# Optimization experiments

Hardware: AMD Instinct MI355X
Metric: run time of the kernel (lower is better)

The kernel has to match this reference:

```python
import jax, jax.numpy as jnp
import numpy as np

BLANK = 0          # tf.nn.ctc_loss default blank_index (StringLookup reserves 0 for OOV)
PAD = 127          # padding_value = char_to_num.vocabulary_size()
NEG = -1e30        # log-space 'zero' (avoid -inf to keep grads NaN-free)
B, T, C, L = 1024, 256, 128, 32


def setup_inputs() -> dict:
    key = jax.random.key(0)
    k1, k2 = jax.random.split(key)
    # labels in [1, PAD-1]; none equal PAD so label_length == L (full-length labels)
    y_true = jax.random.randint(k1, (B, L), 1, PAD).astype(jnp.int32)
    y_pred = jax.random.normal(k2, (B, T, C), dtype=jnp.float32)
    return {"y_true": y_true, "y_pred": y_pred}


def _ctc_loss(y_true, y_pred):
    """Faithful jax version of tf.nn.ctc_loss(labels, logits, label_len, T,
    logits_time_major=False, blank_index=0): standard log-space alpha DP."""
    Bn, Tn, Cn = y_pred.shape
    Ln = y_true.shape[1]
    S = 2 * Ln + 1  # extended label length (blanks interleaved)

    logp = jax.nn.log_softmax(y_pred, axis=-1)                    # [B,T,C]

    # extended label sequence: blank, l1, blank, l2, ..., blank   # [B,S]
    ext = jnp.full((Bn, S), BLANK, dtype=y_true.dtype)
    ext = ext.at[:, 1::2].set(y_true)

    # log-probs gathered at extended-label symbols                # [B,T,S]
    lp_ext = jnp.take_along_axis(
        logp, jnp.broadcast_to(ext[:, None, :], (Bn, Tn, S)), axis=2)

    # label_length = count of non-padding entries (mirrors count_nonzero)
    label_len = jnp.sum(y_true != PAD, axis=1)                    # [B]

    # skip transition s-2 -> s allowed iff ext[s] is a non-blank differing
    # from ext[s-2]
    skip_ok = jnp.concatenate(
        [jnp.zeros((Bn, 2), bool),
         (ext[:, 2:] != BLANK) & (ext[:, 2:] != ext[:, :-2])], axis=1)  # [B,S]

    neg1 = jnp.full((Bn, 1), NEG, logp.dtype)
    neg2 = jnp.full((Bn, 2), NEG, logp.dtype)

    alpha0 = jnp.full((Bn, S), NEG, logp.dtype)
    alpha0 = alpha0.at[:, 0].set(lp_ext[:, 0, 0]).at[:, 1].set(lp_ext[:, 0, 1])

    def step(alpha, lp_t):  # alpha,[B,S]  lp_t,[B,S]
        a1 = jnp.concatenate([neg1, alpha[:, :-1]], axis=1)
        a2 = jnp.concatenate([neg2, alpha[:, :-2]], axis=1)
        a2 = jnp.where(skip_ok, a2, NEG)
        new = lp_t + jnp.logaddexp(jnp.logaddexp(alpha, a1), a2)
        return new, None

    lp_seq = jnp.transpose(lp_ext, (1, 0, 2))                     # [T,B,S]
    alphaT, _ = jax.lax.scan(step, alpha0, lp_seq[1:])            # [B,S]

    # total log-likelihood ends at last blank (2*len) or last label (2*len-1)
    bi = jnp.arange(Bn)
    e1 = 2 * label_len
    e2 = 2 * label_len - 1
    loglik = jnp.logaddexp(alphaT[bi, e1], alphaT[bi, e2])        # [B]
    return -loglik


def reference(y_true, y_pred):
    # The original layer returns y_pred and registers the loss via add_loss;
    # the compute-dominant quantity is the per-example CTC loss, returned here.
    return _ctc_loss(y_true, y_pred)
```

## Files before the change

### kernel.cpp

```cpp
#include <hip/hip_runtime.h>
#include <cstdint>


#define CTC_BLANK 0
#define CTC_PAD   127
#define NEG       (-1e30f)
#define LOG2E     1.44269504088896340736f
#define LN2       0.69314718055994530942f

constexpr int Bn = 1024, Tn = 256, Cn = 128, Ln = 32;
constexpr int NSLOT = Ln + 1;
constexpr int CR  = 8;
constexpr int NCH = Tn / CR;
constexpr int CF  = CR * Cn;

__device__ __forceinline__ float fexp2(float x) { return __builtin_amdgcn_exp2f(x); }
__device__ __forceinline__ float flog2(float x) { return __builtin_amdgcn_logf(x); }

template <int CTRL>
__device__ __forceinline__ float dpp_add(float s) {
    int v = __builtin_amdgcn_update_dpp(0, __float_as_int(s), CTRL, 0xF, 0xF, true);
    return s + __int_as_float(v);
}
__device__ __forceinline__ float dpp_wave_shr1(float src, float old) {
    return __int_as_float(__builtin_amdgcn_update_dpp(
        __float_as_int(old), __float_as_int(src), 0x138, 0xF, 0xF, false));
}
__device__ __forceinline__ void gl_lds16(const float* g, float* l) {
    __builtin_amdgcn_global_load_lds(
        (const __attribute__((address_space(1))) uint32_t*)g,
        (__attribute__((address_space(3))) uint32_t*)l, 16, 0, 0);
}

__global__ __launch_bounds__(256, 6) void ctc_fused_kernel(
        const int*   __restrict__ y_true,
        const float* __restrict__ y_pred,
        float*       __restrict__ out)
{
    __shared__ __align__(16) float raw[2][CF];
    __shared__ _Float16 Gc[Tn * NSLOT];
    __shared__ int   labels[Ln];
    __shared__ __align__(16) int cmap[Cn];
    __shared__ int   wcnt[4];
    __shared__ float partS[16];
    __shared__ float aEs[64], aOs[64];
    int* const used = (int*)raw[1];

    const int b    = blockIdx.x;
    const int tid  = threadIdx.x;
    const int lane = tid & 63;
    const int wave = tid >> 6;
    const int half = lane >> 5;
    const int l32  = lane & 31;
    const int rotb = (b + (b >> 8)) & 3;

    const float* gbase = y_pred + (size_t)b * Tn * Cn;

    auto stage = [&](int c) {
        gl_lds16(gbase + (size_t)(c * CR + 2 * wave) * Cn + lane * 4,
                 &raw[c & 1][wave * 256]);
    };

    stage(0);

    if (tid < Ln) labels[tid] = y_true[b * Ln + tid];
    if (tid < Cn) used[tid] = 0;
    __syncthreads();
    if (tid == 0) used[CTC_BLANK] = 1;
    if (tid < Ln) used[labels[tid]] = 1;
    __syncthreads();
    {
        bool f = (tid < Cn) && (used[tid] != 0);
        unsigned long long m = __ballot(f);
        if (lane == 0) wcnt[wave] = __popcll(m);
        __syncthreads();
        int base = 0;
        for (int w = 0; w < wave; ++w) base += wcnt[w];
        if (tid < Cn)
            cmap[tid] = f ? (base + __popcll(m & ((1ull << lane) - 1ull))) : -1;
        __syncthreads();
    }

    const int4 cm = ((const int4*)cmap)[l32];
    const int rl = 2 * wave + half;
    float accE = 0.f, accO = 0.f;

    const int  i      = lane;
    const bool validO = (i < Ln);
    const bool validE = (i <= Ln);
    const int  myLab   = validO ? labels[i] : -1;
    const int  prevLab = (i >= 1 && i < Ln) ? labels[i - 1] : -1;
    const int  slotO   = validO ? cmap[myLab] : 0;
    const bool skipO   = (i >= 1 && i < Ln) &&
                         (myLab != CTC_BLANK) && (myLab != prevLab);
    const int  len = __popcll(__ballot(validO && (myLab != CTC_PAD)));
    float aE = NEG, aO = NEG;

    auto dp_chunk = [&](int t0, int t1) {
        int t = t0;
        if (t == 0) {
            aE = (i == 0) ? (float)Gc[0]     : NEG;
            aO = (i == 0) ? (float)Gc[slotO] : NEG;
            t = 1;
        } else {
            aE = aEs[i];
            aO = aOs[i];
        }
        float pB[2], pO[2];
        const int ta = t, tb = (t + 1 < t1) ? t + 1 : t1 - 1;
        pB[0] = (float)Gc[ta * NSLOT]; pO[0] = (float)Gc[ta * NSLOT + slotO];
        pB[1] = (float)Gc[tb * NSLOT]; pO[1] = (float)Gc[tb * NSLOT + slotO];
        int k = 0;
        #pragma unroll 2
        for (; t < t1; ++t) {
            const float lpB = pB[k], lpO = pO[k];
            const int tp = (t + 2 < t1) ? t + 2 : t1 - 1;
            pB[k] = (float)Gc[tp * NSLOT];
            pO[k] = (float)Gc[tp * NSLOT + slotO];
            k ^= 1;

            const float aOup = dpp_wave_shr1(aO, NEG);
            const float m  = fmaxf(aE, aOup);
            const float e1 = fexp2(aE - m);
            const float e2 = fexp2(aOup - m);
            const float sE = e1 + e2;
            const float nE = lpB + m + flog2(sE);
            const float m3 = fmaxf(aO, m);
            const float nO = lpO + m3 +
                flog2(fexp2(aO - m3) + (skipO ? sE : e1) * fexp2(m - m3));
            aE = validE ? nE : NEG;
            aO = validO ? nO : NEG;
        }
        aEs[i] = aE;
        aOs[i] = aO;
    };

    auto process = [&](int c, float& acc) {
        const int r = c * CR + rl;
        const float4 x = ((const float4*)&raw[c & 1][wave * 256 + half * 128])[l32];
        const float e0 = x.x * LOG2E, e1 = x.y * LOG2E,
                    e2 = x.z * LOG2E, e3 = x.w * LOG2E;
        if (cm.x >= 0) Gc[r * NSLOT + cm.x] = (_Float16)e0;
        if (cm.y >= 0) Gc[r * NSLOT + cm.y] = (_Float16)e1;
        if (cm.z >= 0) Gc[r * NSLOT + cm.z] = (_Float16)e2;
        if (cm.w >= 0) Gc[r * NSLOT + cm.w] = (_Float16)e3;
        float s = fexp2(e0) + fexp2(e1) + fexp2(e2) + fexp2(e3);
        s = dpp_add<0x111>(s);
        s = dpp_add<0x112>(s);
        s = dpp_add<0x114>(s);
        s = dpp_add<0x118>(s);
        s = dpp_add<0x142>(s);
        acc += flog2(s);
    };

    auto iter = [&](int c, float& acc) {
        if (c + 1 < NCH) stage(c + 1);
        if (c > 0 && wave == ((c - 1 + rotb) & 3))
            dp_chunk((c - 1) * CR, c * CR);
        __builtin_amdgcn_sched_barrier(0);
        if (c + 1 < NCH) asm volatile("s_waitcnt vmcnt(1)" ::: "memory");
        else             asm volatile("s_waitcnt vmcnt(0)" ::: "memory");
        __builtin_amdgcn_sched_barrier(0);
        process(c, acc);
        if (c == NCH - 1 && l32 == 31) {
            partS[rl]     = accE;
            partS[rl + 8] = accO;
        }
        asm volatile("s_waitcnt lgkmcnt(0)" ::: "memory");
        __builtin_amdgcn_s_barrier();
    };

    for (int cc = 0; cc < NCH / 2; ++cc) {
        iter(2 * cc,     accE);
        iter(2 * cc + 1, accO);
    }

    if (wave == ((NCH - 1 + rotb) & 3)) {
        dp_chunk(Tn - CR, Tn);
        const float v1 = __shfl(aE, len, 64);
        const float v2 = __shfl(aO, len - 1, 64);
        if (i == 0) {
            float S = 0.f;
            #pragma unroll
            for (int j = 0; j < 16; ++j) S += partS[j];
            const float mm = fmaxf(v1, v2);
            const float L2 = mm + flog2(fexp2(v1 - mm) + fexp2(v2 - mm));
            out[b] = LN2 * (S - L2);
        }
    }
}

extern "C" void kernel_launch(void* const* d_in, const int* in_sizes, int n_in,
                              void* d_out, int out_size, void* d_ws, size_t ws_size,
                              hipStream_t stream) {
    const int*   y_true = (const int*)d_in[0];
    const float* y_pred = (const float*)d_in[1];
    float*       out    = (float*)d_out;
    ctc_fused_kernel<<<Bn, 256, 0, stream>>>(y_true, y_pred, out);
}
```

Measured before the change: 198.7 us.

## Run CTC alpha recursion in linear space with per-chunk exponent rescaling

The alpha DP switches from log-space logaddexp (max, exp2 and log2 on every step) to plain multiply-adds on exponentiated emission values. After each 8-step chunk, a wave-wide max reduction picks a power-of-two scale, and the accumulated exponent is tracked in shared memory. The final log-likelihood is one log2 plus that exponent. This shortens the serial per-timestep dependency chain. In exchange it relies on float range staying safe within a chunk, adds a cross-lane reduction per chunk, and may change numerics for very small alphas.

```diff
diff --git a/kernel.cpp b/kernel.cpp
--- a/kernel.cpp
+++ b/kernel.cpp
@@ -4,7 +4,6 @@
 
 #define CTC_BLANK 0
 #define CTC_PAD   127
-#define NEG       (-1e30f)
 #define LOG2E     1.44269504088896340736f
 #define LN2       0.69314718055994530942f
 
@@ -44,6 +43,7 @@
     __shared__ int   wcnt[4];
     __shared__ float partS[16];
     __shared__ float aEs[64], aOs[64];
+    __shared__ int   EscS;
     int* const used = (int*)raw[1];
 
     const int b    = blockIdx.x;
@@ -94,45 +94,51 @@
     const bool skipO   = (i >= 1 && i < Ln) &&
                          (myLab != CTC_BLANK) && (myLab != prevLab);
     const int  len = __popcll(__ballot(validO && (myLab != CTC_PAD)));
-    float aE = NEG, aO = NEG;
+    float aE = 0.f, aO = 0.f;
+    int   Esc = 0;
 
     auto dp_chunk = [&](int t0, int t1) {
         int t = t0;
         if (t == 0) {
-            aE = (i == 0) ? (float)Gc[0]     : NEG;
-            aO = (i == 0) ? (float)Gc[slotO] : NEG;
+            aE = (i == 0) ? fexp2((float)Gc[0])     : 0.f;
+            aO = (i == 0) ? fexp2((float)Gc[slotO]) : 0.f;
+            Esc = 0;
             t = 1;
         } else {
-            aE = aEs[i];
-            aO = aOs[i];
+            aE  = aEs[i];
+            aO  = aOs[i];
+            Esc = EscS;
         }
         float pB[2], pO[2];
         const int ta = t, tb = (t + 1 < t1) ? t + 1 : t1 - 1;
-        pB[0] = (float)Gc[ta * NSLOT]; pO[0] = (float)Gc[ta * NSLOT + slotO];
-        pB[1] = (float)Gc[tb * NSLOT]; pO[1] = (float)Gc[tb * NSLOT + slotO];
+        pB[0] = fexp2((float)Gc[ta * NSLOT]);
+        pO[0] = fexp2((float)Gc[ta * NSLOT + slotO]);
+        pB[1] = fexp2((float)Gc[tb * NSLOT]);
+        pO[1] = fexp2((float)Gc[tb * NSLOT + slotO]);
         int k = 0;
         #pragma unroll 2
         for (; t < t1; ++t) {
             const float lpB = pB[k], lpO = pO[k];
             const int tp = (t + 2 < t1) ? t + 2 : t1 - 1;
-            pB[k] = (float)Gc[tp * NSLOT];
-            pO[k] = (float)Gc[tp * NSLOT + slotO];
+            pB[k] = fexp2((float)Gc[tp * NSLOT]);
+            pO[k] = fexp2((float)Gc[tp * NSLOT + slotO]);
             k ^= 1;
 
-            const float aOup = dpp_wave_shr1(aO, NEG);
-            const float m  = fmaxf(aE, aOup);
-            const float e1 = fexp2(aE - m);
-            const float e2 = fexp2(aOup - m);
-            const float sE = e1 + e2;
-            const float nE = lpB + m + flog2(sE);
-            const float m3 = fmaxf(aO, m);
-            const float nO = lpO + m3 +
-                flog2(fexp2(aO - m3) + (skipO ? sE : e1) * fexp2(m - m3));
-            aE = validE ? nE : NEG;
-            aO = validO ? nO : NEG;
-        }
+            const float aOup = dpp_wave_shr1(aO, 0.f);
+            const float nE = lpB * (aE + aOup);
+            const float nO = lpO * (aO + aE + (skipO ? aOup : 0.f));
+            aE = validE ? nE : 0.f;
+            aO = validO ? nO : 0.f;
+        }
+        float m = fmaxf(aE, aO);
+        #pragma unroll
+        for (int d = 1; d < 64; d <<= 1) m = fmaxf(m, __shfl_xor(m, d, 64));
+        const int ex = ((__float_as_int(m) >> 23) & 255) - 127;
+        const float sc = __int_as_float((127 - ex) << 23);
+        aE *= sc; aO *= sc; Esc += ex;
         aEs[i] = aE;
         aOs[i] = aO;
+        if (i == 0) EscS = Esc;
     };
 
     auto process = [&](int c, float& acc) {
@@ -183,8 +189,7 @@
             float S = 0.f;
             #pragma unroll
             for (int j = 0; j < 16; ++j) S += partS[j];
-            const float mm = fmaxf(v1, v2);
-            const float L2 = mm + flog2(fexp2(v1 - mm) + fexp2(v2 - mm));
+            const float L2 = flog2(v1 + v2) + (float)Esc;
             out[b] = LN2 * (S - L2);
         }
     }
```

Result: no change. 195.9 us (-1.4%).
